# Optimization experiments

Hardware: AMD Instinct MI355X
Metric: run time of the kernel (lower is better)

The kernel has to match this reference:

```python
import jax, jax.numpy as jnp
import numpy as np

N_NODES = 50000
N_EDGES = 600000
D_FEAT = 128


def setup_inputs() -> dict:
    key = jax.random.key(0)
    ks = jax.random.split(key, 10)
    x = jax.random.normal(ks[0], (N_NODES, D_FEAT), dtype=jnp.float32)
    src = jax.random.randint(ks[1], (N_EDGES,), 0, N_NODES, dtype=jnp.int32)
    dst = jax.random.randint(ks[2], (N_EDGES,), 0, N_NODES, dtype=jnp.int32)
    w1 = jax.random.normal(ks[3], (1, D_FEAT), dtype=jnp.float32) * 0.05
    Wd1 = jax.random.normal(ks[4], (D_FEAT, 64), dtype=jnp.float32) * 0.05
    b1 = jnp.zeros((64,), dtype=jnp.float32)
    w2 = jax.random.normal(ks[5], (1, 64), dtype=jnp.float32) * 0.05
    Wd2 = jax.random.normal(ks[6], (64, 32), dtype=jnp.float32) * 0.05
    b2 = jnp.zeros((32,), dtype=jnp.float32)
    Wout = jax.random.normal(ks[7], (32, 4), dtype=jnp.float32) * 0.05
    bout = jnp.zeros((4,), dtype=jnp.float32)
    return {"x": x, "src": src, "dst": dst, "w1": w1, "Wd1": Wd1, "b1": b1,
            "w2": w2, "Wd2": Wd2, "b2": b2, "Wout": Wout, "bout": bout}


def _spmm(src, dst, h):
    # A @ h for COO adjacency (edge src -> dst contributes h[src] into row dst)
    return jax.ops.segment_sum(h[src], dst, num_segments=N_NODES)


def reference(x, src, dst, w1, Wd1, b1, w2, Wd2, b2, Wout, bout):
    # input_layer is an Input wrapper: identity. Dropout is identity at inference.
    h = _spmm(src, dst, x) * w1          # GraphLayer 1: SpMM + elementwise scale
    h = h @ Wd1 + b1                     # Dense(64), linear activation
    h = _spmm(src, dst, h) * w2          # GraphLayer 2
    h = h @ Wd2 + b2                     # Dense(32)
    logits = h @ Wout + bout             # Dense(4)
    return jax.nn.softmax(logits, axis=-1)
```

## Files before the change

### kernel.cpp

```cpp
#include <hip/hip_runtime.h>

#define D_FEAT 128
#define NP 64
#define NP_SHIFT 6
#define P_PARTS 782
#define CAP 1024
#define EPB 4096


__global__ __launch_bounds__(256) void fused_xw_bucket_kernel(
    const float4* __restrict__ x4,
    const int* __restrict__ src,
    const int* __restrict__ dst,
    const float* __restrict__ w1,  const float* __restrict__ Wd1,
    const float* __restrict__ b1,  const float* __restrict__ w2,
    const float* __restrict__ Wd2, const float* __restrict__ b2,
    const float* __restrict__ Wout, const float* __restrict__ bout,
    int* __restrict__ partFill, int* __restrict__ edgeBuf,
    float* __restrict__ gc, float4* __restrict__ u4,
    int nN, int nE, int xwBlocks)
{
    __shared__ __align__(16) int sm[2 * P_PARTS];
    int t = threadIdx.x;

    if ((int)blockIdx.x < xwBlocks) {
        float*  T2 = (float*)sm;
        float4* W4 = (float4*)(sm + 256);
        {
            int m = t >> 2, j = t & 3;
            float s = 0.f;
            for (int p = 0; p < 32; ++p) s += Wd2[m * 32 + p] * Wout[p * 4 + j];
            T2[t] = w2[m] * s;
        }
        __syncthreads();
        for (int idx = t; idx < 512; idx += 256) {
            int k = idx >> 2, j = idx & 3;
            float s = 0.f;
            for (int m = 0; m < 64; ++m) s += Wd1[k * 64 + m] * T2[m * 4 + j];
            ((float*)W4)[idx] = w1[k] * s;
        }
        if (blockIdx.x == 0 && t < 4) {
            float s = 0.f;
            for (int m = 0; m < 64; ++m) s += b1[m] * T2[m * 4 + t];
            gc[t] = s;
            float s2 = 0.f;
            for (int p = 0; p < 32; ++p) s2 += b2[p] * Wout[p * 4 + t];
            gc[4 + t] = s2 + bout[t];
        }
        __syncthreads();

        int lane = t & 63;
        int li   = lane & 7;
        int sub  = lane >> 3;
        int wv   = t >> 6;
        float4 wr[4][4];
        #pragma unroll
        for (int q = 0; q < 4; ++q)
            #pragma unroll
            for (int e = 0; e < 4; ++e)
                wr[q][e] = W4[4 * (li + 8 * q) + e];

        int R0 = blockIdx.x * 256;
        #pragma unroll 2
        for (int p = 0; p < 8; ++p) {
            int r = R0 + p * 32 + wv * 8 + sub;
            bool ok = r < nN;
            size_t base = (size_t)r * 32 + li;
            float4 a = make_float4(0.f, 0.f, 0.f, 0.f);
            #pragma unroll
            for (int q = 0; q < 4; ++q) {
                float4 xv = ok ? x4[base + 8 * q]
                               : make_float4(0.f, 0.f, 0.f, 0.f);
                a.x += xv.x*wr[q][0].x + xv.y*wr[q][1].x + xv.z*wr[q][2].x + xv.w*wr[q][3].x;
                a.y += xv.x*wr[q][0].y + xv.y*wr[q][1].y + xv.z*wr[q][2].y + xv.w*wr[q][3].y;
                a.z += xv.x*wr[q][0].z + xv.y*wr[q][1].z + xv.z*wr[q][2].z + xv.w*wr[q][3].z;
                a.w += xv.x*wr[q][0].w + xv.y*wr[q][1].w + xv.z*wr[q][2].w + xv.w*wr[q][3].w;
            }
            #pragma unroll
            for (int m = 4; m >= 1; m >>= 1) {
                a.x += __shfl_xor(a.x, m);
                a.y += __shfl_xor(a.y, m);
                a.z += __shfl_xor(a.z, m);
                a.w += __shfl_xor(a.w, m);
            }
            if (ok && li == 0) u4[r] = a;
        }
    } else {
        int b = blockIdx.x - xwBlocks;
        int* hist = sm;
        int* base = sm + P_PARTS;
        for (int p = t; p < P_PARTS; p += 256) hist[p] = 0;
        __syncthreads();
        int beg = b * EPB;
        int end = min(beg + EPB, nE);
        for (int i4 = (beg >> 2) + t; i4 * 4 < end; i4 += 256) {
            if (i4 * 4 + 3 < end) {
                int4 d4 = ((const int4*)dst)[i4];
                atomicAdd(&hist[d4.x >> NP_SHIFT], 1);
                atomicAdd(&hist[d4.y >> NP_SHIFT], 1);
                atomicAdd(&hist[d4.z >> NP_SHIFT], 1);
                atomicAdd(&hist[d4.w >> NP_SHIFT], 1);
            } else {
                for (int i = i4 * 4; i < end; ++i)
                    atomicAdd(&hist[dst[i] >> NP_SHIFT], 1);
            }
        }
        __syncthreads();
        for (int p = t; p < P_PARTS; p += 256) {
            int h = hist[p];
            base[p] = h ? atomicAdd(&partFill[p], h) : 0;
        }
        __syncthreads();
        for (int i4 = (beg >> 2) + t; i4 * 4 < end; i4 += 256) {
            if (i4 * 4 + 3 < end) {
                int4 d4 = ((const int4*)dst)[i4];
                int4 s4 = ((const int4*)src)[i4];
                int dd[4] = {d4.x, d4.y, d4.z, d4.w};
                int ss[4] = {s4.x, s4.y, s4.z, s4.w};
                #pragma unroll
                for (int j = 0; j < 4; ++j) {
                    int p = dd[j] >> NP_SHIFT;
                    int rank = atomicSub(&hist[p], 1) - 1;
                    int pos = base[p] + rank;
                    if (pos < CAP)
                        edgeBuf[p * CAP + pos] = ss[j] | ((dd[j] & (NP - 1)) << 16);
                }
            } else {
                for (int i = i4 * 4; i < end; ++i) {
                    int d = dst[i];
                    int p = d >> NP_SHIFT;
                    int rank = atomicSub(&hist[p], 1) - 1;
                    int pos = base[p] + rank;
                    if (pos < CAP)
                        edgeBuf[p * CAP + pos] = src[i] | ((d & (NP - 1)) << 16);
                }
            }
        }
    }
}

__global__ __launch_bounds__(256) void spmm_part_kernel(
    const int* __restrict__ partFill,
    const int* __restrict__ edgeBuf,
    const float4* __restrict__ in4,
    const float* __restrict__ gc, int gcOff,
    float4* __restrict__ out4, int nN, int doSoftmax)
{
    __shared__ float acc[4][72];
    int t = threadIdx.x, p = blockIdx.x;
    for (int i = t; i < 288; i += 256) ((float*)acc)[i] = 0.f;
    __syncthreads();
    int n = min(partFill[p], CAP);
    int4 e4 = ((const int4*)(edgeBuf + p * CAP))[t];
    int b0 = 4 * t;
    {
        int ee[4] = {e4.x, e4.y, e4.z, e4.w};
        #pragma unroll
        for (int j = 0; j < 4; ++j) {
            if (b0 + j < n) {
                int e = ee[j];
                float4 val = in4[e & 0xFFFF];
                int dl = e >> 16;
                atomicAdd(&acc[0][dl], val.x);
                atomicAdd(&acc[1][dl], val.y);
                atomicAdd(&acc[2][dl], val.z);
                atomicAdd(&acc[3][dl], val.w);
            }
        }
    }
    __syncthreads();
    if (t < NP) {
        int node = p * NP + t;
        if (node < nN) {
            float lx = acc[0][t] + gc[gcOff + 0];
            float ly = acc[1][t] + gc[gcOff + 1];
            float lz = acc[2][t] + gc[gcOff + 2];
            float lw = acc[3][t] + gc[gcOff + 3];
            if (doSoftmax) {
                float m = fmaxf(fmaxf(lx, ly), fmaxf(lz, lw));
                float ex = __expf(lx - m);
                float ey = __expf(ly - m);
                float ez = __expf(lz - m);
                float ew = __expf(lw - m);
                float r = 1.f / (ex + ey + ez + ew);
                out4[node] = make_float4(ex * r, ey * r, ez * r, ew * r);
            } else {
                out4[node] = make_float4(lx, ly, lz, lw);
            }
        }
    }
}

extern "C" void kernel_launch(void* const* d_in, const int* in_sizes, int n_in,
                              void* d_out, int out_size, void* d_ws, size_t ws_size,
                              hipStream_t stream)
{
    const float* x    = (const float*)d_in[0];
    const int*   src  = (const int*)d_in[1];
    const int*   dst  = (const int*)d_in[2];
    const float* w1   = (const float*)d_in[3];
    const float* Wd1  = (const float*)d_in[4];
    const float* b1   = (const float*)d_in[5];
    const float* w2   = (const float*)d_in[6];
    const float* Wd2  = (const float*)d_in[7];
    const float* b2   = (const float*)d_in[8];
    const float* Wout = (const float*)d_in[9];
    const float* bout = (const float*)d_in[10];

    const int nE = in_sizes[1];
    const int nN = in_sizes[0] / D_FEAT;

    float* ws = (float*)d_ws;
    float* gc = ws;
    float* u  = ws + 16;
    float* v  = u + (size_t)nN * 4;
    int* partFill = (int*)(v + (size_t)nN * 4);
    int* edgeBuf  = partFill + ((P_PARTS + 63) & ~63);

    const int xwBlocks = (nN + 255) / 256;
    const int bkBlocks = (nE + EPB - 1) / EPB;

    hipMemsetAsync(partFill, 0, P_PARTS * sizeof(int), stream);
    fused_xw_bucket_kernel<<<xwBlocks + bkBlocks, 256, 0, stream>>>(
        (const float4*)x, src, dst, w1, Wd1, b1, w2, Wd2, b2, Wout, bout,
        partFill, edgeBuf, gc, (float4*)u, nN, nE, xwBlocks);
    spmm_part_kernel<<<P_PARTS, 256, 0, stream>>>(partFill, edgeBuf,
                                                  (const float4*)u, gc, 0,
                                                  (float4*)v, nN, 0);
    spmm_part_kernel<<<P_PARTS, 256, 0, stream>>>(partFill, edgeBuf,
                                                  (const float4*)v, gc, 4,
                                                  (float4*)d_out, nN, 1);
}
```

Before: 150.8 us.

## Fuse all stages into one persistent kernel with software grid barriers

Merges the projection/bucketing kernel and both SpMM kernels into a single kernel of 782 blocks, one per 64-node partition. Software grid barriers on global atomics replace the kernel boundaries, which removes two launches and the gaps between them. During the first SpMM each block also builds a per-destination sorted source list in shared memory and reuses it for the second SpMM, which becomes an atomic-free gather-reduce. Other changes: EPB shrinks so each block buckets exactly one chunk of edges, and partFill counters are padded to avoid contention. The scheme depends on all 782 blocks being co-resident (launch bounds request 4 blocks per SM), otherwise the spin barrier can deadlock or time out.

```diff
diff --git a/kernel.cpp b/kernel.cpp
--- a/kernel.cpp
+++ b/kernel.cpp
@@ -5,187 +5,243 @@
 #define NP_SHIFT 6
 #define P_PARTS 782
 #define CAP 1024
-#define EPB 4096
-
-
-__global__ __launch_bounds__(256) void fused_xw_bucket_kernel(
+#define EPB 768
+#define PF_STRIDE 16
+
+
+__device__ __forceinline__ float4 f4add(float4 a, float4 b) {
+    return make_float4(a.x + b.x, a.y + b.y, a.z + b.z, a.w + b.w);
+}
+
+__device__ __forceinline__ void grid_sync(int* __restrict__ bar, int slot, int nB)
+{
+    __syncthreads();
+    if (threadIdx.x == 0) {
+        __threadfence();
+        __hip_atomic_fetch_add(&bar[slot * 16], 1, __ATOMIC_RELEASE,
+                               __HIP_MEMORY_SCOPE_AGENT);
+        int guard = 0;
+        while (__hip_atomic_load(&bar[slot * 16], __ATOMIC_ACQUIRE,
+                                 __HIP_MEMORY_SCOPE_AGENT) < nB) {
+            if (++guard > (1 << 28)) break;
+        }
+    }
+    __syncthreads();
+    __threadfence();
+}
+
+__global__ __launch_bounds__(256, 4) void mega_kernel(
     const float4* __restrict__ x4,
-    const int* __restrict__ src,
-    const int* __restrict__ dst,
-    const float* __restrict__ w1,  const float* __restrict__ Wd1,
-    const float* __restrict__ b1,  const float* __restrict__ w2,
+    const int* __restrict__ src, const int* __restrict__ dst,
+    const float* __restrict__ w1, const float* __restrict__ Wd1,
+    const float* __restrict__ b1, const float* __restrict__ w2,
     const float* __restrict__ Wd2, const float* __restrict__ b2,
     const float* __restrict__ Wout, const float* __restrict__ bout,
-    int* __restrict__ partFill, int* __restrict__ edgeBuf,
-    float* __restrict__ gc, float4* __restrict__ u4,
-    int nN, int nE, int xwBlocks)
+    int* __restrict__ bar, int* __restrict__ partFill,
+    int* __restrict__ edgeBuf, float* __restrict__ gc,
+    float4* __restrict__ u4, float4* __restrict__ v4,
+    float4* __restrict__ out4, int nN, int nE)
 {
-    __shared__ __align__(16) int sm[2 * P_PARTS];
-    int t = threadIdx.x;
-
-    if ((int)blockIdx.x < xwBlocks) {
-        float*  T2 = (float*)sm;
-        float4* W4 = (float4*)(sm + 256);
-        {
-            int m = t >> 2, j = t & 3;
-            float s = 0.f;
-            for (int p = 0; p < 32; ++p) s += Wd2[m * 32 + p] * Wout[p * 4 + j];
-            T2[t] = w2[m] * s;
-        }
-        __syncthreads();
-        for (int idx = t; idx < 512; idx += 256) {
-            int k = idx >> 2, j = idx & 3;
-            float s = 0.f;
-            for (int m = 0; m < 64; ++m) s += Wd1[k * 64 + m] * T2[m * 4 + j];
-            ((float*)W4)[idx] = w1[k] * s;
-        }
-        if (blockIdx.x == 0 && t < 4) {
-            float s = 0.f;
-            for (int m = 0; m < 64; ++m) s += b1[m] * T2[m * 4 + t];
-            gc[t] = s;
-            float s2 = 0.f;
-            for (int p = 0; p < 32; ++p) s2 += b2[p] * Wout[p * 4 + t];
-            gc[4 + t] = s2 + bout[t];
-        }
-        __syncthreads();
-
-        int lane = t & 63;
-        int li   = lane & 7;
-        int sub  = lane >> 3;
-        int wv   = t >> 6;
+    __shared__ union {
+        struct { float T2[256]; float4 W4[128]; } a;
+        struct { int hist[P_PARTS]; int base[P_PARTS]; } k;
+        struct { float acc[4][72]; int hist64[64];
+                 int off[65]; int sorted[CAP]; } b;
+    } sm;
+
+    const int t = threadIdx.x;
+    const int p = blockIdx.x;
+
+    {
+        int m = t >> 2, j = t & 3;
+        float s = 0.f;
+        for (int q = 0; q < 32; ++q) s += Wd2[m * 32 + q] * Wout[q * 4 + j];
+        sm.a.T2[t] = w2[m] * s;
+    }
+    __syncthreads();
+    for (int idx = t; idx < 512; idx += 256) {
+        int k = idx >> 2, j = idx & 3;
+        float s = 0.f;
+        for (int m = 0; m < 64; ++m) s += Wd1[k * 64 + m] * sm.a.T2[m * 4 + j];
+        ((float*)sm.a.W4)[idx] = w1[k] * s;
+    }
+    if (p == 0 && t < 4) {
+        float s = 0.f;
+        for (int m = 0; m < 64; ++m) s += b1[m] * sm.a.T2[m * 4 + t];
+        gc[t] = s;
+        float s2 = 0.f;
+        for (int q = 0; q < 32; ++q) s2 += b2[q] * Wout[q * 4 + t];
+        gc[4 + t] = s2 + bout[t];
+    }
+    __syncthreads();
+
+    {
+        int lane = t & 63, li = lane & 7, sb = lane >> 3, wv = t >> 6;
         float4 wr[4][4];
         #pragma unroll
         for (int q = 0; q < 4; ++q)
             #pragma unroll
             for (int e = 0; e < 4; ++e)
-                wr[q][e] = W4[4 * (li + 8 * q) + e];
-
-        int R0 = blockIdx.x * 256;
-        #pragma unroll 2
-        for (int p = 0; p < 8; ++p) {
-            int r = R0 + p * 32 + wv * 8 + sub;
+                wr[q][e] = sm.a.W4[4 * (li + 8 * q) + e];
+        int R0 = p * NP;
+        #pragma unroll
+        for (int ps = 0; ps < 2; ++ps) {
+            int r = R0 + ps * 32 + wv * 8 + sb;
             bool ok = r < nN;
             size_t base = (size_t)r * 32 + li;
             float4 a = make_float4(0.f, 0.f, 0.f, 0.f);
             #pragma unroll
             for (int q = 0; q < 4; ++q) {
-                float4 xv = ok ? x4[base + 8 * q]
-                               : make_float4(0.f, 0.f, 0.f, 0.f);
+                float4 xv = ok ? x4[base + 8 * q] : make_float4(0.f, 0.f, 0.f, 0.f);
                 a.x += xv.x*wr[q][0].x + xv.y*wr[q][1].x + xv.z*wr[q][2].x + xv.w*wr[q][3].x;
                 a.y += xv.x*wr[q][0].y + xv.y*wr[q][1].y + xv.z*wr[q][2].y + xv.w*wr[q][3].y;
                 a.z += xv.x*wr[q][0].z + xv.y*wr[q][1].z + xv.z*wr[q][2].z + xv.w*wr[q][3].z;
                 a.w += xv.x*wr[q][0].w + xv.y*wr[q][1].w + xv.z*wr[q][2].w + xv.w*wr[q][3].w;
             }
             #pragma unroll
-            for (int m = 4; m >= 1; m >>= 1) {
-                a.x += __shfl_xor(a.x, m);
-                a.y += __shfl_xor(a.y, m);
-                a.z += __shfl_xor(a.z, m);
-                a.w += __shfl_xor(a.w, m);
+            for (int msk = 4; msk >= 1; msk >>= 1) {
+                a.x += __shfl_xor(a.x, msk);
+                a.y += __shfl_xor(a.y, msk);
+                a.z += __shfl_xor(a.z, msk);
+                a.w += __shfl_xor(a.w, msk);
             }
             if (ok && li == 0) u4[r] = a;
         }
-    } else {
-        int b = blockIdx.x - xwBlocks;
-        int* hist = sm;
-        int* base = sm + P_PARTS;
-        for (int p = t; p < P_PARTS; p += 256) hist[p] = 0;
-        __syncthreads();
-        int beg = b * EPB;
-        int end = min(beg + EPB, nE);
-        for (int i4 = (beg >> 2) + t; i4 * 4 < end; i4 += 256) {
-            if (i4 * 4 + 3 < end) {
-                int4 d4 = ((const int4*)dst)[i4];
-                atomicAdd(&hist[d4.x >> NP_SHIFT], 1);
-                atomicAdd(&hist[d4.y >> NP_SHIFT], 1);
-                atomicAdd(&hist[d4.z >> NP_SHIFT], 1);
-                atomicAdd(&hist[d4.w >> NP_SHIFT], 1);
-            } else {
-                for (int i = i4 * 4; i < end; ++i)
-                    atomicAdd(&hist[dst[i] >> NP_SHIFT], 1);
-            }
-        }
-        __syncthreads();
-        for (int p = t; p < P_PARTS; p += 256) {
-            int h = hist[p];
-            base[p] = h ? atomicAdd(&partFill[p], h) : 0;
-        }
-        __syncthreads();
-        for (int i4 = (beg >> 2) + t; i4 * 4 < end; i4 += 256) {
-            if (i4 * 4 + 3 < end) {
-                int4 d4 = ((const int4*)dst)[i4];
-                int4 s4 = ((const int4*)src)[i4];
-                int dd[4] = {d4.x, d4.y, d4.z, d4.w};
-                int ss[4] = {s4.x, s4.y, s4.z, s4.w};
-                #pragma unroll
-                for (int j = 0; j < 4; ++j) {
-                    int p = dd[j] >> NP_SHIFT;
-                    int rank = atomicSub(&hist[p], 1) - 1;
-                    int pos = base[p] + rank;
+    }
+    __syncthreads();
+
+    for (int q = t; q < P_PARTS; q += 256) sm.k.hist[q] = 0;
+    __syncthreads();
+    {
+        int beg = p * EPB;
+        int i0  = beg + 4 * t;
+        int4 ed = make_int4(0, 0, 0, 0), es = make_int4(0, 0, 0, 0);
+        bool act  = (4 * t < EPB) && (i0 < nE);
+        bool full = act && (i0 + 3 < nE);
+        if (full) {
+            ed = ((const int4*)dst)[(beg >> 2) + t];
+            es = ((const int4*)src)[(beg >> 2) + t];
+        } else if (act) {
+            for (int j = 0; j < 4 && i0 + j < nE; ++j) {
+                ((int*)&ed)[j] = dst[i0 + j];
+                ((int*)&es)[j] = src[i0 + j];
+            }
+        }
+        int dd[4] = {ed.x, ed.y, ed.z, ed.w};
+        int ss[4] = {es.x, es.y, es.z, es.w};
+        if (act) {
+            #pragma unroll
+            for (int j = 0; j < 4; ++j)
+                if (i0 + j < nE) atomicAdd(&sm.k.hist[dd[j] >> NP_SHIFT], 1);
+        }
+        __syncthreads();
+        for (int q = t; q < P_PARTS; q += 256) {
+            int h = sm.k.hist[q];
+            sm.k.base[q] = h ? atomicAdd(&partFill[q * PF_STRIDE], h) : 0;
+        }
+        __syncthreads();
+        if (act) {
+            #pragma unroll
+            for (int j = 0; j < 4; ++j) {
+                if (i0 + j < nE) {
+                    int d = dd[j], pp = d >> NP_SHIFT;
+                    int rank = atomicSub(&sm.k.hist[pp], 1) - 1;
+                    int pos = sm.k.base[pp] + rank;
                     if (pos < CAP)
-                        edgeBuf[p * CAP + pos] = ss[j] | ((dd[j] & (NP - 1)) << 16);
+                        edgeBuf[pp * CAP + pos] = ss[j] | ((d & (NP - 1)) << 16);
                 }
-            } else {
-                for (int i = i4 * 4; i < end; ++i) {
-                    int d = dst[i];
-                    int p = d >> NP_SHIFT;
-                    int rank = atomicSub(&hist[p], 1) - 1;
-                    int pos = base[p] + rank;
-                    if (pos < CAP)
-                        edgeBuf[p * CAP + pos] = src[i] | ((d & (NP - 1)) << 16);
-                }
-            }
-        }
-    }
-}
-
-__global__ __launch_bounds__(256) void spmm_part_kernel(
-    const int* __restrict__ partFill,
-    const int* __restrict__ edgeBuf,
-    const float4* __restrict__ in4,
-    const float* __restrict__ gc, int gcOff,
-    float4* __restrict__ out4, int nN, int doSoftmax)
-{
-    __shared__ float acc[4][72];
-    int t = threadIdx.x, p = blockIdx.x;
-    for (int i = t; i < 288; i += 256) ((float*)acc)[i] = 0.f;
-    __syncthreads();
-    int n = min(partFill[p], CAP);
-    int4 e4 = ((const int4*)(edgeBuf + p * CAP))[t];
-    int b0 = 4 * t;
-    {
-        int ee[4] = {e4.x, e4.y, e4.z, e4.w};
-        #pragma unroll
-        for (int j = 0; j < 4; ++j) {
-            if (b0 + j < n) {
-                int e = ee[j];
-                float4 val = in4[e & 0xFFFF];
-                int dl = e >> 16;
-                atomicAdd(&acc[0][dl], val.x);
-                atomicAdd(&acc[1][dl], val.y);
-                atomicAdd(&acc[2][dl], val.z);
-                atomicAdd(&acc[3][dl], val.w);
-            }
-        }
-    }
-    __syncthreads();
-    if (t < NP) {
-        int node = p * NP + t;
-        if (node < nN) {
-            float lx = acc[0][t] + gc[gcOff + 0];
-            float ly = acc[1][t] + gc[gcOff + 1];
-            float lz = acc[2][t] + gc[gcOff + 2];
-            float lw = acc[3][t] + gc[gcOff + 3];
-            if (doSoftmax) {
+            }
+        }
+    }
+
+    grid_sync(bar, 0, P_PARTS);
+
+    float4 gv = ((const float4*)gc)[0];
+    float4 cv = ((const float4*)gc)[1];
+    for (int i = t; i < 288; i += 256) ((float*)sm.b.acc)[i] = 0.f;
+    if (t < 64) sm.b.hist64[t] = 0;
+    __syncthreads();
+    {
+        int n = min(partFill[p * PF_STRIDE], CAP);
+        int4 e4 = ((const int4*)(edgeBuf + p * CAP))[t];
+        int b0 = 4 * t;
+        int sA = min(e4.x & 0xFFFF, nN - 1), dA = (e4.x >> 16) & 63;
+        int sB = min(e4.y & 0xFFFF, nN - 1), dB = (e4.y >> 16) & 63;
+        int sC = min(e4.z & 0xFFFF, nN - 1), dC = (e4.z >> 16) & 63;
+        int sD = min(e4.w & 0xFFFF, nN - 1), dD = (e4.w >> 16) & 63;
+        float4 z = make_float4(0.f, 0.f, 0.f, 0.f);
+        float4 gA = (b0 + 0 < n) ? u4[sA] : z;
+        float4 gB = (b0 + 1 < n) ? u4[sB] : z;
+        float4 gC = (b0 + 2 < n) ? u4[sC] : z;
+        float4 gD = (b0 + 3 < n) ? u4[sD] : z;
+        int rA = -1, rB = -1, rC = -1, rD = -1;
+        if (b0 + 0 < n) {
+            rA = atomicAdd(&sm.b.hist64[dA], 1);
+            atomicAdd(&sm.b.acc[0][dA], gA.x); atomicAdd(&sm.b.acc[1][dA], gA.y);
+            atomicAdd(&sm.b.acc[2][dA], gA.z); atomicAdd(&sm.b.acc[3][dA], gA.w);
+        }
+        if (b0 + 1 < n) {
+            rB = atomicAdd(&sm.b.hist64[dB], 1);
+            atomicAdd(&sm.b.acc[0][dB], gB.x); atomicAdd(&sm.b.acc[1][dB], gB.y);
+            atomicAdd(&sm.b.acc[2][dB], gB.z); atomicAdd(&sm.b.acc[3][dB], gB.w);
+        }
+        if (b0 + 2 < n) {
+            rC = atomicAdd(&sm.b.hist64[dC], 1);
+            atomicAdd(&sm.b.acc[0][dC], gC.x); atomicAdd(&sm.b.acc[1][dC], gC.y);
+            atomicAdd(&sm.b.acc[2][dC], gC.z); atomicAdd(&sm.b.acc[3][dC], gC.w);
+        }
+        if (b0 + 3 < n) {
+            rD = atomicAdd(&sm.b.hist64[dD], 1);
+            atomicAdd(&sm.b.acc[0][dD], gD.x); atomicAdd(&sm.b.acc[1][dD], gD.y);
+            atomicAdd(&sm.b.acc[2][dD], gD.z); atomicAdd(&sm.b.acc[3][dD], gD.w);
+        }
+        __syncthreads();
+        if (t < 64) {
+            int xv = sm.b.hist64[t];
+            #pragma unroll
+            for (int d = 1; d < 64; d <<= 1) {
+                int y = __shfl_up(xv, d);
+                if (t >= d) xv += y;
+            }
+            sm.b.off[t + 1] = xv;
+            if (t == 0) sm.b.off[0] = 0;
+        } else if (t < 128) {
+            int dl = t - 64, node = p * NP + dl;
+            if (node < nN) {
+                float4 a = make_float4(sm.b.acc[0][dl], sm.b.acc[1][dl],
+                                       sm.b.acc[2][dl], sm.b.acc[3][dl]);
+                v4[node] = f4add(a, gv);
+            }
+        }
+        __syncthreads();
+        if (rA >= 0) sm.b.sorted[sm.b.off[dA] + rA] = sA;
+        if (rB >= 0) sm.b.sorted[sm.b.off[dB] + rB] = sB;
+        if (rC >= 0) sm.b.sorted[sm.b.off[dC] + rC] = sC;
+        if (rD >= 0) sm.b.sorted[sm.b.off[dD] + rD] = sD;
+    }
+
+    grid_sync(bar, 1, P_PARTS);
+
+    {
+        int dl = t >> 2, sb = t & 3;
+        int lo = sm.b.off[dl], hi = sm.b.off[dl + 1];
+        float4 a = make_float4(0.f, 0.f, 0.f, 0.f);
+        for (int i = lo + sb; i < hi; i += 4)
+            a = f4add(a, v4[sm.b.sorted[i]]);
+        a.x += __shfl_xor(a.x, 1); a.x += __shfl_xor(a.x, 2);
+        a.y += __shfl_xor(a.y, 1); a.y += __shfl_xor(a.y, 2);
+        a.z += __shfl_xor(a.z, 1); a.z += __shfl_xor(a.z, 2);
+        a.w += __shfl_xor(a.w, 1); a.w += __shfl_xor(a.w, 2);
+        if (sb == 0) {
+            int node = p * NP + dl;
+            if (node < nN) {
+                float lx = a.x + cv.x, ly = a.y + cv.y;
+                float lz = a.z + cv.z, lw = a.w + cv.w;
                 float m = fmaxf(fmaxf(lx, ly), fmaxf(lz, lw));
-                float ex = __expf(lx - m);
-                float ey = __expf(ly - m);
-                float ez = __expf(lz - m);
-                float ew = __expf(lw - m);
+                float ex = __expf(lx - m), ey = __expf(ly - m);
+                float ez = __expf(lz - m), ew = __expf(lw - m);
                 float r = 1.f / (ex + ey + ez + ew);
                 out4[node] = make_float4(ex * r, ey * r, ez * r, ew * r);
-            } else {
-                out4[node] = make_float4(lx, ly, lz, lw);
             }
         }
     }
@@ -214,20 +270,14 @@
     float* gc = ws;
     float* u  = ws + 16;
     float* v  = u + (size_t)nN * 4;
-    int* partFill = (int*)(v + (size_t)nN * 4);
-    int* edgeBuf  = partFill + ((P_PARTS + 63) & ~63);
-
-    const int xwBlocks = (nN + 255) / 256;
-    const int bkBlocks = (nE + EPB - 1) / EPB;
-
-    hipMemsetAsync(partFill, 0, P_PARTS * sizeof(int), stream);
-    fused_xw_bucket_kernel<<<xwBlocks + bkBlocks, 256, 0, stream>>>(
+    int* bar      = (int*)(v + (size_t)nN * 4);
+    int* partFill = bar + 64;
+    int* edgeBuf  = partFill + P_PARTS * PF_STRIDE;
+
+    hipMemsetAsync(bar, 0, (64 + P_PARTS * PF_STRIDE) * sizeof(int), stream);
+
+    mega_kernel<<<P_PARTS, 256, 0, stream>>>(
         (const float4*)x, src, dst, w1, Wd1, b1, w2, Wd2, b2, Wout, bout,
-        partFill, edgeBuf, gc, (float4*)u, nN, nE, xwBlocks);
-    spmm_part_kernel<<<P_PARTS, 256, 0, stream>>>(partFill, edgeBuf,
-                                                  (const float4*)u, gc, 0,
-                                                  (float4*)v, nN, 0);
-    spmm_part_kernel<<<P_PARTS, 256, 0, stream>>>(partFill, edgeBuf,
-                                                  (const float4*)v, gc, 4,
-                                                  (float4*)d_out, nN, 1);
-}
+        bar, partFill, edgeBuf, gc, (float4*)u, (float4*)v,
+        (float4*)d_out, nN, nE);
+}
```

Result: slower. 441.1 us (+192.5%).
